# Kernel tuning notes

Hardware: AMD Instinct MI355X
Metric: run time of the kernel (lower is better)

The kernel has to match this reference:

```python
import jax, jax.numpy as jnp
import numpy as np

NUM_HEADS = 8
LN_EPS = 1e-5


def _layernorm(x, g, b):
    m = jnp.mean(x, axis=-1, keepdims=True)
    v = jnp.mean(jnp.square(x - m), axis=-1, keepdims=True)
    return (x - m) * jax.lax.rsqrt(v + LN_EPS) * g + b


def setup_inputs() -> dict:
    key = jax.random.key(0)
    ks = jax.random.split(key, 10)
    D, C, Cin = 2, 256, 64  # depth, embed dim, input channels
    w = lambda k, shape: jax.random.normal(k, shape, jnp.float32) * 0.02
    return {
        "x": jax.random.normal(ks[0], (4, Cin, 12, 12, 12), jnp.float32),
        "W_pe": w(ks[1], (Cin, C)),
        "b_pe": jnp.zeros((C,), jnp.float32),
        "cls_token": w(ks[2], (1, 1, C)),
        "ln1_g": jnp.ones((D, C), jnp.float32),
        "ln1_b": jnp.zeros((D, C), jnp.float32),
        "Wqkv": w(ks[3], (D, C, 3 * C)),
        "Wproj": w(ks[4], (D, C, C)),
        "bproj": jnp.zeros((D, C), jnp.float32),
        "ln2_g": jnp.ones((D, C), jnp.float32),
        "ln2_b": jnp.zeros((D, C), jnp.float32),
        "W1": w(ks[5], (D, C, C)),
        "b1": jnp.zeros((D, C), jnp.float32),
        "W2": w(ks[6], (D, C, C)),
        "b2": jnp.zeros((D, C), jnp.float32),
        "normf_g": jnp.ones((C,), jnp.float32),
        "normf_b": jnp.zeros((C,), jnp.float32),
    }


def reference(x, W_pe, b_pe, cls_token, ln1_g, ln1_b, Wqkv, Wproj, bproj,
              ln2_g, ln2_b, W1, b1, W2, b2, normf_g, normf_b):
    B, Cin, H, W, L = x.shape
    C = W_pe.shape[1]
    hd = C // NUM_HEADS
    scale = hd ** (-0.5)

    # PatchEmbed: 1x1x1 Conv3d == per-voxel linear projection, then flatten to tokens
    tok = jnp.einsum('bchwl,cd->bhwld', x, W_pe).reshape(B, H * W * L, C) + b_pe
    cls = jnp.broadcast_to(cls_token, (B, 1, C))
    t = jnp.concatenate([cls, tok], axis=1)  # [B, N, C], N = H*W*L + 1
    N = t.shape[1]

    depth = Wqkv.shape[0]
    for i in range(depth):
        # --- self-attention ---
        y = _layernorm(t, ln1_g[i], ln1_b[i])
        qkv = (y @ Wqkv[i]).reshape(B, N, 3, NUM_HEADS, hd)
        qkv = jnp.transpose(qkv, (2, 0, 3, 1, 4))  # [3, B, H, N, hd]
        q, k, v = qkv[0], qkv[1], qkv[2]
        attn = jnp.einsum('bhnd,bhmd->bhnm', q, k) * scale
        attn = jax.nn.softmax(attn, axis=-1)
        o = jnp.einsum('bhnm,bhmd->bhnd', attn, v)
        o = jnp.transpose(o, (0, 2, 1, 3)).reshape(B, N, C)
        t = t + (o @ Wproj[i] + bproj[i])
        # --- MLP (mlp_ratio=1.0, exact GELU) ---
        y = _layernorm(t, ln2_g[i], ln2_b[i])
        h = jax.nn.gelu(y @ W1[i] + b1[i], approximate=False)
        t = t + (h @ W2[i] + b2[i])

    t = _layernorm(t, normf_g, normf_b)
    x_cls = t[:, 0]                                   # [B, C]
    feat = t[:, 1:]                                   # [B, H*W*L, C]
    feat = jnp.transpose(feat, (0, 2, 1)).reshape(B, C, H, W, L)  # downsample = Identity for dim=256
    return x_cls, feat
```

## Files before the change

kernel.cpp:

```cpp
#include <hip/hip_runtime.h>
#include <hip/hip_bf16.h>
#include <math.h>

#define B_   4
#define CIN  64
#define P_   1728
#define N_   1729
#define C_   256
#define NH_  8
#define HD_  32
#define M_   (B_*N_)
#define NPAD 1792
#define NB_EMBED 6916

typedef __bf16 bf16x8 __attribute__((ext_vector_type(8)));
typedef __bf16 bf16x4 __attribute__((ext_vector_type(4)));
typedef float  f32x4  __attribute__((ext_vector_type(4)));
typedef float  f32x16 __attribute__((ext_vector_type(16)));

__global__ __launch_bounds__(256) void embed3(
    const float* __restrict__ x, const float* __restrict__ Wpe,
    const float* __restrict__ bpe, const float* __restrict__ cls,
    float* __restrict__ t, __bf16* __restrict__ kB, __bf16* __restrict__ vB,
    float* __restrict__ stats)
{
    if (blockIdx.x >= NB_EMBED) {
        int ex = blockIdx.x - NB_EMBED;
        if (ex < 252) {
            int idx = ex*256 + threadIdx.x;
            if (idx < 32*63*32) {
                int d  = idx & 31;
                int n  = (idx >> 5) % 63 + N_;
                int bh = idx / (63*32);
                kB[((size_t)bh*NPAD + n)*32 + d] = (__bf16)0.f;
                vB[((size_t)bh*32 + d)*NPAD + n] = (__bf16)0.f;
            }
        } else {
            int si = (ex - 252)*256 + threadIdx.x;
            if (si < 2*M_) stats[si] = 0.f;
        }
        return;
    }
    int idx = blockIdx.x*256 + threadIdx.x;
    int c   = idx & 255;
    int n   = (idx >> 8) % N_;
    int b   = idx / (N_*256);
    if (n == 0) { t[idx] = cls[c]; return; }
    int p = n - 1;
    float acc = bpe[c];
    for (int ci = 0; ci < CIN; ++ci)
        acc += x[(size_t)(b*CIN + ci)*P_ + p] * Wpe[ci*C_ + c];
    t[idx] = acc;
}

__global__ __launch_bounds__(256) void ln4(
    const float* __restrict__ in, __bf16* __restrict__ out,
    const float* __restrict__ g, const float* __restrict__ bb)
{
    int wv = threadIdx.x >> 6, lane = threadIdx.x & 63;
    size_t row = (size_t)blockIdx.x*4 + wv;
    float4 v = *(const float4*)&in[row*C_ + lane*4];
    float s1 = (v.x+v.y)+(v.z+v.w);
    float s2 = (v.x*v.x+v.y*v.y)+(v.z*v.z+v.w*v.w);
    #pragma unroll
    for (int off = 32; off >= 1; off >>= 1) {
        s1 += __shfl_xor(s1, off);
        s2 += __shfl_xor(s2, off);
    }
    float mean = s1*(1.0f/C_);
    float var  = fmaxf(s2*(1.0f/C_) - mean*mean, 0.0f);
    float rstd = rsqrtf(var + 1e-5f);
    float4 gg = *(const float4*)&g[lane*4];
    float4 bv = *(const float4*)&bb[lane*4];
    bf16x4 r;
    r[0] = (__bf16)((v.x-mean)*rstd*gg.x + bv.x);
    r[1] = (__bf16)((v.y-mean)*rstd*gg.y + bv.y);
    r[2] = (__bf16)((v.z-mean)*rstd*gg.z + bv.z);
    r[3] = (__bf16)((v.w-mean)*rstd*gg.w + bv.w);
    *(bf16x4*)&out[row*C_ + lane*4] = r;
}

__global__ __launch_bounds__(256) void wprep2(
    const float* __restrict__ Wqkv, const float* __restrict__ Wproj,
    const float* __restrict__ W1,   const float* __restrict__ W2,
    __bf16* __restrict__ wT)
{
    int z = blockIdx.z, which = z >> 1, layer = z & 1;
    const float* src; __bf16* dst; int NC;
    if (which == 0) {
        src = Wqkv + (size_t)layer*C_*768;
        dst = wT   + (size_t)layer*768*256;
        NC  = 768;
    } else {
        NC = 256;
        const float* b3 = (which == 1) ? Wproj : (which == 2) ? W1 : W2;
        src = b3 + (size_t)layer*65536;
        dst = wT + 2*768*256 + (size_t)((which-1)*2 + layer)*65536;
    }
    int n0 = blockIdx.x*32; if (n0 >= NC) return;
    int k0 = blockIdx.y*32;
    __shared__ float tile[32][33];
    int c = threadIdx.x & 31, r = threadIdx.x >> 5;
    for (int rr = r; rr < 32; rr += 8)
        tile[rr][c] = src[(size_t)(k0+rr)*NC + n0 + c];
    __syncthreads();
    for (int rr = r; rr < 32; rr += 8)
        dst[(size_t)(n0+rr)*256 + k0 + c] = (__bf16)tile[c][rr];
}

template<int NC, bool ADD, bool GELU, bool BIAS, bool OUTBF, bool STATS>
__global__ __launch_bounds__(256) void gemm4(
    const __bf16* __restrict__ A, const __bf16* __restrict__ Wt,
    const float* __restrict__ bias, float* __restrict__ outF,
    __bf16* __restrict__ outB, float* __restrict__ stats)
{
    __shared__ __align__(16) __bf16 As[2][64*64];
    __shared__ __align__(16) __bf16 Bs[2][64*64];
    int r0 = blockIdx.x*64, c0 = blockIdx.y*64;
    int tid = threadIdx.x;
    int wv = tid >> 6, lane = tid & 63, quad = lane >> 4, mn = lane & 15;
    int sr = tid >> 2, sc = tid & 3;
    int ga = r0 + sr; if (ga >= M_) ga = M_ - 1;

    f32x4 acc[4];
    #pragma unroll
    for (int ct = 0; ct < 4; ++ct)
        #pragma unroll
        for (int rr = 0; rr < 4; ++rr) acc[ct][rr] = 0.f;

    bf16x8 ra0, ra1, rb0, rb1;
#define GLOAD(KC) do {                                                   \
        ra0 = *(const bf16x8*)&A[(size_t)ga*256 + (KC)*64 + sc*8];       \
        ra1 = *(const bf16x8*)&A[(size_t)ga*256 + (KC)*64 + sc*8 + 32];  \
        rb0 = *(const bf16x8*)&Wt[(size_t)(c0+sr)*256 + (KC)*64 + sc*8]; \
        rb1 = *(const bf16x8*)&Wt[(size_t)(c0+sr)*256 + (KC)*64 + sc*8 + 32]; \
    } while (0)
#define SSTORE(BUF) do {                                                 \
        *(bf16x8*)&As[BUF][sr*64 + ((sc ^ (sr & 7))*8)]       = ra0;     \
        *(bf16x8*)&As[BUF][sr*64 + (((sc+4) ^ (sr & 7))*8)]   = ra1;     \
        *(bf16x8*)&Bs[BUF][sr*64 + ((sc ^ (sr & 7))*8)]       = rb0;     \
        *(bf16x8*)&Bs[BUF][sr*64 + (((sc+4) ^ (sr & 7))*8)]   = rb1;     \
    } while (0)

    GLOAD(0);
    SSTORE(0);
    __syncthreads();

    for (int kc = 0; kc < 4; ++kc) {
        int cur = kc & 1;
        if (kc < 3) GLOAD(kc+1);
        __builtin_amdgcn_sched_barrier(0);

        #pragma unroll
        for (int h = 0; h < 2; ++h) {
            bf16x8 a = *(const bf16x8*)&As[cur][(wv*16 + mn)*64 + (((h*4+quad) ^ (mn & 7))*8)];
            #pragma unroll
            for (int ct = 0; ct < 4; ++ct) {
                bf16x8 b = *(const bf16x8*)&Bs[cur][(ct*16 + mn)*64 + (((h*4+quad) ^ (mn & 7))*8)];
                acc[ct] = __builtin_amdgcn_mfma_f32_16x16x32_bf16(a, b, acc[ct], 0, 0, 0);
            }
        }

        if (kc < 3) {
            SSTORE(cur^1);
            __syncthreads();
        }
    }
#undef GLOAD
#undef SSTORE

    float rs1[4] = {0.f,0.f,0.f,0.f}, rs2[4] = {0.f,0.f,0.f,0.f};
    #pragma unroll
    for (int ct = 0; ct < 4; ++ct) {
        int col = c0 + ct*16 + mn;
        #pragma unroll
        for (int rr = 0; rr < 4; ++rr) {
            int row = r0 + wv*16 + quad*4 + rr;
            if (row >= M_) continue;
            float val = acc[ct][rr];
            if (BIAS) val += bias[col];
            if (GELU) val = 0.5f*val*(1.f + erff(val*0.70710678118654752f));
            size_t oi = (size_t)row*NC + col;
            if (OUTBF) outB[oi] = (__bf16)val;
            else if (ADD) {
                float tv = outF[oi] + val;
                outF[oi] = tv;
                if (STATS) { rs1[rr] += tv; rs2[rr] += tv*tv; }
            }
            else outF[oi] = val;
        }
    }
    if (STATS) {
        #pragma unroll
        for (int rr = 0; rr < 4; ++rr) {
            float s1 = rs1[rr], s2 = rs2[rr];
            s1 += __shfl_xor(s1, 1); s1 += __shfl_xor(s1, 2);
            s1 += __shfl_xor(s1, 4); s1 += __shfl_xor(s1, 8);
            s2 += __shfl_xor(s2, 1); s2 += __shfl_xor(s2, 2);
            s2 += __shfl_xor(s2, 4); s2 += __shfl_xor(s2, 8);
            int row = r0 + wv*16 + quad*4 + rr;
            if (mn == 0 && row < M_) {
                atomicAdd(&stats[2*row],     s1);
                atomicAdd(&stats[2*row + 1], s2);
            }
        }
    }
}

__global__ __launch_bounds__(256) void gemm_qkv4(
    const __bf16* __restrict__ A, const __bf16* __restrict__ Wt,
    __bf16* __restrict__ qB, __bf16* __restrict__ kB, __bf16* __restrict__ vB)
{
    __shared__ __align__(16) __bf16 As[2][64*64];
    __shared__ __align__(16) __bf16 Bs[2][64*64];
    int r0 = blockIdx.x*64, c0 = blockIdx.y*64;
    int tid = threadIdx.x;
    int wv = tid >> 6, lane = tid & 63, quad = lane >> 4, mn = lane & 15;
    int sr = tid >> 2, sc = tid & 3;
    int ga = r0 + sr; if (ga >= M_) ga = M_ - 1;

    f32x4 acc[4];
    #pragma unroll
    for (int ct = 0; ct < 4; ++ct)
        #pragma unroll
        for (int rr = 0; rr < 4; ++rr) acc[ct][rr] = 0.f;

    bf16x8 ra0, ra1, rb0, rb1;
#define GLOAD(KC) do {                                                   \
        ra0 = *(const bf16x8*)&A[(size_t)ga*256 + (KC)*64 + sc*8];       \
        ra1 = *(const bf16x8*)&A[(size_t)ga*256 + (KC)*64 + sc*8 + 32];  \
        rb0 = *(const bf16x8*)&Wt[(size_t)(c0+sr)*256 + (KC)*64 + sc*8]; \
        rb1 = *(const bf16x8*)&Wt[(size_t)(c0+sr)*256 + (KC)*64 + sc*8 + 32]; \
    } while (0)
#define SSTORE(BUF) do {                                                 \
        *(bf16x8*)&As[BUF][sr*64 + ((sc ^ (sr & 7))*8)]       = ra0;     \
        *(bf16x8*)&As[BUF][sr*64 + (((sc+4) ^ (sr & 7))*8)]   = ra1;     \
        *(bf16x8*)&Bs[BUF][sr*64 + ((sc ^ (sr & 7))*8)]       = rb0;     \
        *(bf16x8*)&Bs[BUF][sr*64 + (((sc+4) ^ (sr & 7))*8)]   = rb1;     \
    } while (0)

    GLOAD(0);
    SSTORE(0);
    __syncthreads();

    for (int kc = 0; kc < 4; ++kc) {
        int cur = kc & 1;
        if (kc < 3) GLOAD(kc+1);
        __builtin_amdgcn_sched_barrier(0);

        #pragma unroll
        for (int h = 0; h < 2; ++h) {
            bf16x8 a = *(const bf16x8*)&As[cur][(wv*16 + mn)*64 + (((h*4+quad) ^ (mn & 7))*8)];
            #pragma unroll
            for (int ct = 0; ct < 4; ++ct) {
                bf16x8 b = *(const bf16x8*)&Bs[cur][(ct*16 + mn)*64 + (((h*4+quad) ^ (mn & 7))*8)];
                acc[ct] = __builtin_amdgcn_mfma_f32_16x16x32_bf16(a, b, acc[ct], 0, 0, 0);
            }
        }

        if (kc < 3) {
            SSTORE(cur^1);
            __syncthreads();
        }
    }
#undef GLOAD
#undef SSTORE

    const float scale = 0.2550348727f;
    #pragma unroll
    for (int ct = 0; ct < 4; ++ct) {
        int col = c0 + ct*16 + mn;
        #pragma unroll
        for (int rr = 0; rr < 4; ++rr) {
            int row = r0 + wv*16 + quad*4 + rr;
            if (row >= M_) continue;
            int b = row / N_, n = row - b*N_;
            float val = acc[ct][rr];
            if (col < 256) {
                int h = col >> 5, dd = col & 31;
                qB[((size_t)(b*NH_+h)*NPAD + n)*32 + dd] = (__bf16)(val*scale);
            } else if (col < 512) {
                int h = (col-256) >> 5, dd = col & 31;
                kB[((size_t)(b*NH_+h)*NPAD + n)*32 + dd] = (__bf16)val;
            } else {
                int h = (col-512) >> 5, dd = col & 31;
                vB[((size_t)(b*NH_+h)*32 + dd)*NPAD + n] = (__bf16)val;
            }
        }
    }
}

#define LKS 40
#define LVS 136

__device__ __forceinline__ float fexp2(float x) {
    float r; asm("v_exp_f32 %0, %1" : "=v"(r) : "v"(x)); return r;
}
__device__ __forceinline__ unsigned cvtpk_bf16(float lo, float hi) {
    unsigned r;
    asm("v_cvt_pk_bf16_f32 %0, %1, %2" : "=v"(r) : "v"(lo), "v"(hi));
    return r;
}

__global__ __launch_bounds__(256) void attn16(
    const __bf16* __restrict__ qB, const __bf16* __restrict__ kB,
    const __bf16* __restrict__ vB, __bf16* __restrict__ o)
{
    int bh = blockIdx.x, b = bh >> 3, h = bh & 7;
    int q0 = blockIdx.y * 128;
    int tid = threadIdx.x;
    int wv = tid >> 6, lane = tid & 63, lo5 = lane & 31, hi = lane >> 5;

    __shared__ __align__(16) __bf16 lk[2][128*LKS];
    __shared__ __align__(16) __bf16 lvt[2][32*LVS];

    const __bf16* kbase = kB + (size_t)bh*NPAD*32;
    const __bf16* vbase = vB + (size_t)bh*32*NPAD;

    const __bf16* qrow = qB + ((size_t)bh*NPAD + q0 + wv*32 + lo5)*32 + hi*8;
    bf16x8 qf0 = *(const bf16x8*)(qrow);
    bf16x8 qf1 = *(const bf16x8*)(qrow + 16);

    f32x16 oaccA, oaccB;
    #pragma unroll
    for (int r = 0; r < 16; ++r) { oaccA[r] = 0.f; oaccB[r] = 0.f; }
    float lsum = 0.f;

    int sr2 = tid >> 1, hc = tid & 1;
    int vr = tid >> 3, vc = tid & 7;

    bf16x8 ks0, ks1, vs0, vs1;
#define ATTN_LOAD(T) do {                                              \
        const __bf16* kp_ = kbase + ((size_t)((T)*128 + sr2))*32 + hc*16; \
        ks0 = *(const bf16x8*)(kp_);                                   \
        ks1 = *(const bf16x8*)(kp_ + 8);                               \
        const __bf16* vp_ = vbase + (size_t)vr*NPAD + (T)*128 + vc*16; \
        vs0 = *(const bf16x8*)(vp_);                                   \
        vs1 = *(const bf16x8*)(vp_ + 8);                               \
    } while (0)
#define ATTN_STORE(BUF) do {                                           \
        __bf16* kd = &lk[BUF][sr2*LKS + hc*16];                        \
        *(bf16x8*)(kd)     = ks0;  *(bf16x8*)(kd + 8) = ks1;           \
        __bf16* vd = &lvt[BUF][vr*LVS + vc*16];                        \
        *(bf16x8*)(vd)     = vs0;  *(bf16x8*)(vd + 8) = vs1;           \
    } while (0)

    ATTN_LOAD(0);
    ATTN_STORE(0);
    __syncthreads();

    for (int t = 0; t < 14; ++t) {
        int cur = t & 1;
        if (t < 13) ATTN_LOAD(t+1);
        __builtin_amdgcn_sched_barrier(0);

        f32x16 s[4];
        __builtin_amdgcn_s_setprio(1);
        #pragma unroll
        for (int kg = 0; kg < 4; ++kg) {
            const __bf16* kf = &lk[cur][(kg*32 + lo5)*LKS + hi*8];
            bf16x8 kf0 = *(const bf16x8*)(kf);
            bf16x8 kf1 = *(const bf16x8*)(kf + 16);
            #pragma unroll
            for (int r = 0; r < 16; ++r) s[kg][r] = 0.f;
            s[kg] = __builtin_amdgcn_mfma_f32_32x32x16_bf16(kf0, qf0, s[kg], 0, 0, 0);
            s[kg] = __builtin_amdgcn_mfma_f32_32x32x16_bf16(kf1, qf1, s[kg], 0, 0, 0);
        }
        __builtin_amdgcn_s_setprio(0);

        #pragma unroll
        for (int kg = 0; kg < 4; ++kg) {
            float p[16];
            #pragma unroll
            for (int r = 0; r < 16; ++r) p[r] = fexp2(s[kg][r]);
            float l0 = 0.f, l1 = 0.f;
            #pragma unroll
            for (int r = 0; r < 8; ++r) { l0 += p[r]; l1 += p[r+8]; }
            lsum += l0 + l1;

            unsigned a0 = cvtpk_bf16(p[0],  p[1]),  a1 = cvtpk_bf16(p[2],  p[3]);
            unsigned b0 = cvtpk_bf16(p[4],  p[5]),  b1 = cvtpk_bf16(p[6],  p[7]);
            unsigned c0 = cvtpk_bf16(p[8],  p[9]),  c1 = cvtpk_bf16(p[10], p[11]);
            unsigned d0 = cvtpk_bf16(p[12], p[13]), d1 = cvtpk_bf16(p[14], p[15]);
            asm("v_permlane32_swap_b32 %0, %1" : "+v"(a0), "+v"(b0));
            asm("v_permlane32_swap_b32 %0, %1" : "+v"(a1), "+v"(b1));
            asm("v_permlane32_swap_b32 %0, %1" : "+v"(c0), "+v"(d0));
            asm("v_permlane32_swap_b32 %0, %1" : "+v"(c1), "+v"(d1));
            union { bf16x8 v; unsigned u[4]; } f0, f1;
            f0.u[0] = a0; f0.u[1] = a1; f0.u[2] = b0; f0.u[3] = b1;
            f1.u[0] = c0; f1.u[1] = c1; f1.u[2] = d0; f1.u[3] = d1;

            const __bf16* vf = &lvt[cur][lo5*LVS + kg*32 + hi*8];
            bf16x8 vf0 = *(const bf16x8*)(vf);
            bf16x8 vf1 = *(const bf16x8*)(vf + 16);
            __builtin_amdgcn_s_setprio(1);
            if (kg & 1) {
                oaccB = __builtin_amdgcn_mfma_f32_32x32x16_bf16(f0.v, vf0, oaccB, 0, 0, 0);
                oaccB = __builtin_amdgcn_mfma_f32_32x32x16_bf16(f1.v, vf1, oaccB, 0, 0, 0);
            } else {
                oaccA = __builtin_amdgcn_mfma_f32_32x32x16_bf16(f0.v, vf0, oaccA, 0, 0, 0);
                oaccA = __builtin_amdgcn_mfma_f32_32x32x16_bf16(f1.v, vf1, oaccA, 0, 0, 0);
            }
            __builtin_amdgcn_s_setprio(0);
        }

        if (t < 13) {
            ATTN_STORE(cur^1);
            __syncthreads();
        }
    }
#undef ATTN_LOAD
#undef ATTN_STORE

    lsum += __shfl_xor(lsum, 32);
    float inv = 1.0f / (lsum - 63.0f);

    #pragma unroll
    for (int r = 0; r < 16; ++r) {
        float oa = oaccA[r] + oaccB[r];
        int qrw = (r & 3) + 8*(r >> 2) + 4*hi;
        float li = __shfl(inv, qrw);
        int q = q0 + wv*32 + qrw;
        if (q < N_)
            o[((size_t)b*N_ + q)*C_ + h*HD_ + lo5] = (__bf16)(oa * li);
    }
}

__global__ __launch_bounds__(256) void featln(
    const float* __restrict__ t, const float* __restrict__ stats,
    const float* __restrict__ g, const float* __restrict__ bb,
    float* __restrict__ out_cls, float* __restrict__ out_feat)
{
    int bx = blockIdx.x;
    if (bx == 54) {
        if (blockIdx.y != 0) return;
        int b = blockIdx.z, c = threadIdx.x;
        size_t row = (size_t)b*N_;
        float s1 = stats[2*row], s2 = stats[2*row+1];
        float mean = s1*(1.0f/C_);
        float rstd = rsqrtf(fmaxf(s2*(1.0f/C_) - mean*mean, 0.0f) + 1e-5f);
        out_cls[b*C_ + c] = (t[row*C_ + c] - mean)*rstd*g[c] + bb[c];
        return;
    }
    __shared__ float tl[32][33];
    int p0 = bx*32, c0 = blockIdx.y*32, b = blockIdx.z;
    int cc = threadIdx.x & 31, rr = threadIdx.x >> 5;
    float gg = g[c0+cc], bv = bb[c0+cc];
    for (int i = rr; i < 32; i += 8) {
        size_t row = (size_t)b*N_ + 1 + p0 + i;
        float s1 = stats[2*row], s2 = stats[2*row+1];
        float mean = s1*(1.0f/C_);
        float rstd = rsqrtf(fmaxf(s2*(1.0f/C_) - mean*mean, 0.0f) + 1e-5f);
        tl[i][cc] = (t[row*C_ + c0 + cc] - mean)*rstd*gg + bv;
    }
    __syncthreads();
    for (int i = rr; i < 32; i += 8)
        out_feat[((size_t)(b*C_) + c0 + i)*P_ + p0 + cc] = tl[cc][i];
}

extern "C" void kernel_launch(void* const* d_in, const int* in_sizes, int n_in,
                              void* d_out, int out_size, void* d_ws, size_t ws_size,
                              hipStream_t stream)
{
    const float* x        = (const float*)d_in[0];
    const float* W_pe     = (const float*)d_in[1];
    const float* b_pe     = (const float*)d_in[2];
    const float* cls_tok  = (const float*)d_in[3];
    const float* ln1_g    = (const float*)d_in[4];
    const float* ln1_b    = (const float*)d_in[5];
    const float* Wqkv     = (const float*)d_in[6];
    const float* Wproj    = (const float*)d_in[7];
    const float* bproj    = (const float*)d_in[8];
    const float* ln2_g    = (const float*)d_in[9];
    const float* ln2_b    = (const float*)d_in[10];
    const float* W1       = (const float*)d_in[11];
    const float* b1       = (const float*)d_in[12];
    const float* W2       = (const float*)d_in[13];
    const float* b2       = (const float*)d_in[14];
    const float* normf_g  = (const float*)d_in[15];
    const float* normf_b  = (const float*)d_in[16];

    const size_t MC = (size_t)M_*C_;
    float*  ws  = (float*)d_ws;
    float*  t   = ws;
    float*  stats = ws + MC;
    __bf16* ybf = (__bf16*)(ws + 2*MC);
    __bf16* hbf = (__bf16*)(ws + 2*MC + MC/2);
    __bf16* obf = (__bf16*)(ws + 2*MC + MC);
    __bf16* wT  = (__bf16*)(ws + 2*MC + 3*(MC/2));
    __bf16* qB  = wT + 2*768*256 + 6*256*256;
    __bf16* kB  = qB + (size_t)B_*NH_*NPAD*32;
    __bf16* vB  = kB + (size_t)B_*NH_*NPAD*32;

    __bf16* projT = wT + 2*768*256;
    __bf16* w1T   = projT + 2*256*256;
    __bf16* w2T   = w1T   + 2*256*256;

    float* out_cls  = (float*)d_out;
    float* out_feat = out_cls + B_*C_;

    wprep2<<<dim3(24, 8, 8), 256, 0, stream>>>(Wqkv, Wproj, W1, W2, wT);
    embed3<<<NB_EMBED + 252 + 55, 256, 0, stream>>>(
        x, W_pe, b_pe, cls_tok, t, kB, vB, stats);

    const int GRID_M = (M_ + 63) / 64;
    for (int i = 0; i < 2; ++i) {
        ln4<<<M_/4, 256, 0, stream>>>(t, ybf, ln1_g + i*C_, ln1_b + i*C_);
        gemm_qkv4<<<dim3(GRID_M, 12), 256, 0, stream>>>(
            ybf, wT + (size_t)i*768*256, qB, kB, vB);
        attn16<<<dim3(32, 14), 256, 0, stream>>>(qB, kB, vB, obf);
        gemm4<256,true,false,true,false,false><<<dim3(GRID_M, 4), 256, 0, stream>>>(
            obf, projT + (size_t)i*65536, bproj + i*C_, t, nullptr, nullptr);
        ln4<<<M_/4, 256, 0, stream>>>(t, ybf, ln2_g + i*C_, ln2_b + i*C_);
        gemm4<256,false,true,true,true,false><<<dim3(GRID_M, 4), 256, 0, stream>>>(
            ybf, w1T + (size_t)i*65536, b1 + i*C_, nullptr, hbf, nullptr);
        if (i == 0)
            gemm4<256,true,false,true,false,false><<<dim3(GRID_M, 4), 256, 0, stream>>>(
                hbf, w2T + (size_t)i*65536, b2 + i*C_, t, nullptr, nullptr);
        else
            gemm4<256,true,false,true,false,true><<<dim3(GRID_M, 4), 256, 0, stream>>>(
                hbf, w2T + (size_t)i*65536, b2 + i*C_, t, nullptr, stats);
    }

    featln<<<dim3(55, 8, 4), 256, 0, stream>>>(
        t, stats, normf_g, normf_b, out_cls, out_feat);
}
```

Measured before the change: 277.6 us.

## Stage V tile through LDS for coalesced stores; double attention block size

The QKV GEMM now stages V-column accumulators in shared memory (reusing the operand buffers) so the transposed V layout is written with contiguous rows instead of strided scattered bf16 stores. The attention kernel moves to 512-thread blocks covering 256 queries each, so every K/V tile loaded into LDS serves twice as many query rows and fewer blocks are launched. The price is fewer, larger attention blocks (224 of them), which lowers occupancy and parallelism, plus an extra barrier pair in V-column GEMM blocks.

```diff
diff --git a/kernel.cpp b/kernel.cpp
--- a/kernel.cpp
+++ b/kernel.cpp
@@ -207,12 +207,11 @@
     }
 }
 
-__global__ __launch_bounds__(256) void gemm_qkv4(
+__global__ __launch_bounds__(256) void gemm_qkv7(
     const __bf16* __restrict__ A, const __bf16* __restrict__ Wt,
     __bf16* __restrict__ qB, __bf16* __restrict__ kB, __bf16* __restrict__ vB)
 {
-    __shared__ __align__(16) __bf16 As[2][64*64];
-    __shared__ __align__(16) __bf16 Bs[2][64*64];
+    __shared__ __align__(16) __bf16 ABs[4][64*64];
     int r0 = blockIdx.x*64, c0 = blockIdx.y*64;
     int tid = threadIdx.x;
     int wv = tid >> 6, lane = tid & 63, quad = lane >> 4, mn = lane & 15;
@@ -233,10 +232,10 @@
         rb1 = *(const bf16x8*)&Wt[(size_t)(c0+sr)*256 + (KC)*64 + sc*8 + 32]; \
     } while (0)
 #define SSTORE(BUF) do {                                                 \
-        *(bf16x8*)&As[BUF][sr*64 + ((sc ^ (sr & 7))*8)]       = ra0;     \
-        *(bf16x8*)&As[BUF][sr*64 + (((sc+4) ^ (sr & 7))*8)]   = ra1;     \
-        *(bf16x8*)&Bs[BUF][sr*64 + ((sc ^ (sr & 7))*8)]       = rb0;     \
-        *(bf16x8*)&Bs[BUF][sr*64 + (((sc+4) ^ (sr & 7))*8)]   = rb1;     \
+        *(bf16x8*)&ABs[BUF][sr*64 + ((sc ^ (sr & 7))*8)]       = ra0;    \
+        *(bf16x8*)&ABs[BUF][sr*64 + (((sc+4) ^ (sr & 7))*8)]   = ra1;    \
+        *(bf16x8*)&ABs[2+(BUF)][sr*64 + ((sc ^ (sr & 7))*8)]     = rb0;  \
+        *(bf16x8*)&ABs[2+(BUF)][sr*64 + (((sc+4) ^ (sr & 7))*8)] = rb1;  \
     } while (0)
 
     GLOAD(0);
@@ -250,10 +249,10 @@
 
         #pragma unroll
         for (int h = 0; h < 2; ++h) {
-            bf16x8 a = *(const bf16x8*)&As[cur][(wv*16 + mn)*64 + (((h*4+quad) ^ (mn & 7))*8)];
+            bf16x8 a = *(const bf16x8*)&ABs[cur][(wv*16 + mn)*64 + (((h*4+quad) ^ (mn & 7))*8)];
             #pragma unroll
             for (int ct = 0; ct < 4; ++ct) {
-                bf16x8 b = *(const bf16x8*)&Bs[cur][(ct*16 + mn)*64 + (((h*4+quad) ^ (mn & 7))*8)];
+                bf16x8 b = *(const bf16x8*)&ABs[2+cur][(ct*16 + mn)*64 + (((h*4+quad) ^ (mn & 7))*8)];
                 acc[ct] = __builtin_amdgcn_mfma_f32_16x16x32_bf16(a, b, acc[ct], 0, 0, 0);
             }
         }
@@ -267,25 +266,45 @@
 #undef SSTORE
 
     const float scale = 0.2550348727f;
-    #pragma unroll
-    for (int ct = 0; ct < 4; ++ct) {
-        int col = c0 + ct*16 + mn;
-        #pragma unroll
-        for (int rr = 0; rr < 4; ++rr) {
-            int row = r0 + wv*16 + quad*4 + rr;
+    if (c0 < 512) {
+        #pragma unroll
+        for (int ct = 0; ct < 4; ++ct) {
+            int col = c0 + ct*16 + mn;
+            #pragma unroll
+            for (int rr = 0; rr < 4; ++rr) {
+                int row = r0 + wv*16 + quad*4 + rr;
+                if (row >= M_) continue;
+                int b = row / N_, n = row - b*N_;
+                float val = acc[ct][rr];
+                if (col < 256) {
+                    int h = col >> 5, dd = col & 31;
+                    qB[((size_t)(b*NH_+h)*NPAD + n)*32 + dd] = (__bf16)(val*scale);
+                } else {
+                    int h = (col-256) >> 5, dd = col & 31;
+                    kB[((size_t)(b*NH_+h)*NPAD + n)*32 + dd] = (__bf16)val;
+                }
+            }
+        }
+    } else {
+        __syncthreads();
+        float* vt = (float*)ABs;
+        #pragma unroll
+        for (int ct = 0; ct < 4; ++ct) {
+            int lc = ct*16 + mn;
+            #pragma unroll
+            for (int rr = 0; rr < 4; ++rr)
+                vt[lc*68 + wv*16 + quad*4 + rr] = acc[ct][rr];
+        }
+        __syncthreads();
+        int lc = tid >> 2, nc = (tid & 3)*16;
+        int colg = c0 + lc;
+        int h = (colg - 512) >> 5, dd = colg & 31;
+        #pragma unroll
+        for (int j = 0; j < 16; ++j) {
+            int row = r0 + nc + j;
             if (row >= M_) continue;
             int b = row / N_, n = row - b*N_;
-            float val = acc[ct][rr];
-            if (col < 256) {
-                int h = col >> 5, dd = col & 31;
-                qB[((size_t)(b*NH_+h)*NPAD + n)*32 + dd] = (__bf16)(val*scale);
-            } else if (col < 512) {
-                int h = (col-256) >> 5, dd = col & 31;
-                kB[((size_t)(b*NH_+h)*NPAD + n)*32 + dd] = (__bf16)val;
-            } else {
-                int h = (col-512) >> 5, dd = col & 31;
-                vB[((size_t)(b*NH_+h)*32 + dd)*NPAD + n] = (__bf16)val;
-            }
+            vB[((size_t)((b*NH_+h)*32 + dd))*NPAD + n] = (__bf16)vt[lc*68 + nc + j];
         }
     }
 }
@@ -302,12 +321,12 @@
     return r;
 }
 
-__global__ __launch_bounds__(256) void attn16(
+__global__ __launch_bounds__(512) void attn17(
     const __bf16* __restrict__ qB, const __bf16* __restrict__ kB,
     const __bf16* __restrict__ vB, __bf16* __restrict__ o)
 {
     int bh = blockIdx.x, b = bh >> 3, h = bh & 7;
-    int q0 = blockIdx.y * 128;
+    int q0 = blockIdx.y * 256;
     int tid = threadIdx.x;
     int wv = tid >> 6, lane = tid & 63, lo5 = lane & 31, hi = lane >> 5;
 
@@ -326,23 +345,17 @@
     for (int r = 0; r < 16; ++r) { oaccA[r] = 0.f; oaccB[r] = 0.f; }
     float lsum = 0.f;
 
-    int sr2 = tid >> 1, hc = tid & 1;
-    int vr = tid >> 3, vc = tid & 7;
-
-    bf16x8 ks0, ks1, vs0, vs1;
+    int ksr = tid >> 2, ksc = tid & 3;
+    int vr  = tid >> 4, vc  = tid & 15;
+
+    bf16x8 ks0, vs0;
 #define ATTN_LOAD(T) do {                                              \
-        const __bf16* kp_ = kbase + ((size_t)((T)*128 + sr2))*32 + hc*16; \
-        ks0 = *(const bf16x8*)(kp_);                                   \
-        ks1 = *(const bf16x8*)(kp_ + 8);                               \
-        const __bf16* vp_ = vbase + (size_t)vr*NPAD + (T)*128 + vc*16; \
-        vs0 = *(const bf16x8*)(vp_);                                   \
-        vs1 = *(const bf16x8*)(vp_ + 8);                               \
+        ks0 = *(const bf16x8*)(kbase + ((size_t)((T)*128 + ksr))*32 + ksc*8); \
+        vs0 = *(const bf16x8*)(vbase + (size_t)vr*NPAD + (T)*128 + vc*8);     \
     } while (0)
 #define ATTN_STORE(BUF) do {                                           \
-        __bf16* kd = &lk[BUF][sr2*LKS + hc*16];                        \
-        *(bf16x8*)(kd)     = ks0;  *(bf16x8*)(kd + 8) = ks1;           \
-        __bf16* vd = &lvt[BUF][vr*LVS + vc*16];                        \
-        *(bf16x8*)(vd)     = vs0;  *(bf16x8*)(vd + 8) = vs1;           \
+        *(bf16x8*)&lk[BUF][ksr*LKS + ksc*8] = ks0;                     \
+        *(bf16x8*)&lvt[BUF][vr*LVS + vc*8]  = vs0;                     \
     } while (0)
 
     ATTN_LOAD(0);
@@ -506,9 +519,9 @@
     const int GRID_M = (M_ + 63) / 64;
     for (int i = 0; i < 2; ++i) {
         ln4<<<M_/4, 256, 0, stream>>>(t, ybf, ln1_g + i*C_, ln1_b + i*C_);
-        gemm_qkv4<<<dim3(GRID_M, 12), 256, 0, stream>>>(
+        gemm_qkv7<<<dim3(GRID_M, 12), 256, 0, stream>>>(
             ybf, wT + (size_t)i*768*256, qB, kB, vB);
-        attn16<<<dim3(32, 14), 256, 0, stream>>>(qB, kB, vB, obf);
+        attn17<<<dim3(32, 7), 512, 0, stream>>>(qB, kB, vB, obf);
         gemm4<256,true,false,true,false,false><<<dim3(GRID_M, 4), 256, 0, stream>>>(
             obf, projT + (size_t)i*65536, bproj + i*C_, t, nullptr, nullptr);
         ln4<<<M_/4, 256, 0, stream>>>(t, ybf, ln2_g + i*C_, ln2_b + i*C_);
```

New measurement: 266.4 us. 1.04x faster.
